# Performance work log

Measured on AMD Instinct MI355X. Metric: run time of the kernel, lower is better.

## Reference

```python
import jax, jax.numpy as jnp
import numpy as np

D_MODEL = 768
EXPAND = 2
D_STATE = 128
HEADDIM = 64
D_CONV = 4
D_INNER = EXPAND * D_MODEL            # 1536
NHEADS = D_INNER // HEADDIM           # 24
CONV_DIM = D_INNER + 2 * D_STATE      # 1792
D_IN_PROJ = 2 * D_INNER + 2 * D_STATE + NHEADS  # 3352
EPS = 1e-5
BATCH, SEQLEN = 2, 2048


def silu(v):
    return v * jax.nn.sigmoid(v)


def mamba2(x, in_w, conv_w, conv_b, dt_bias, A_log, Dp, norm_w, out_w):
    # x: (b, l, d_model)
    b, l, _ = x.shape
    zxbcdt = x @ in_w.T                              # (b, l, d_in_proj)
    z = zxbcdt[..., :D_INNER]
    xBC = zxbcdt[..., D_INNER:D_INNER + CONV_DIM]
    dt = jax.nn.softplus(zxbcdt[..., D_INNER + CONV_DIM:] + dt_bias)  # (b, l, h)
    # causal depthwise conv1d, kernel D_CONV, left padding D_CONV-1
    pad = jnp.pad(xBC, ((0, 0), (D_CONV - 1, 0), (0, 0)))
    conv = conv_b
    for k in range(D_CONV):
        conv = conv + pad[:, k:k + l, :] * conv_w[:, k]
    xBC = silu(conv)
    xh = xBC[..., :D_INNER].reshape(b, l, NHEADS, HEADDIM)   # (b,l,h,p)
    Bm = xBC[..., D_INNER:D_INNER + D_STATE]                 # (b,l,n) ngroups=1
    Cm = xBC[..., D_INNER + D_STATE:]                        # (b,l,n)
    A = -jnp.exp(A_log)                                      # (h,)
    dA = jnp.exp(dt * A)                                     # (b,l,h)

    def step(h, inp):
        dA_t, dt_t, x_t, B_t, C_t = inp
        # h: (b, h, p, n)
        h = h * dA_t[:, :, None, None] + (dt_t[:, :, None] * x_t)[..., None] * B_t[:, None, None, :]
        y = jnp.einsum('bhpn,bn->bhp', h, C_t)
        return h, y

    h0 = jnp.zeros((b, NHEADS, HEADDIM, D_STATE), x.dtype)
    xs = (dA.transpose(1, 0, 2), dt.transpose(1, 0, 2), xh.transpose(1, 0, 2, 3),
          Bm.transpose(1, 0, 2), Cm.transpose(1, 0, 2))
    _, ys = jax.lax.scan(step, h0, xs)                       # (l,b,h,p)
    y = ys.transpose(1, 0, 2, 3) + Dp[None, None, :, None] * xh
    y = y.reshape(b, l, D_INNER)
    # RMSNormGated (norm_before_gate=False): rmsnorm(y * silu(z)) * weight
    y = y * silu(z)
    y = y * jax.lax.rsqrt(jnp.mean(jnp.square(y), axis=-1, keepdims=True) + EPS) * norm_w
    return y @ out_w.T


def setup_inputs() -> dict:
    key = jax.random.key(0)
    ks = jax.random.split(key, 9)
    s = 0.02
    return {
        'x': jax.random.normal(ks[0], (BATCH, SEQLEN, D_MODEL), jnp.float32),
        'in_proj_w': jax.random.normal(ks[1], (2, D_IN_PROJ, D_MODEL), jnp.float32) * s,
        'conv_w': jax.random.normal(ks[2], (2, CONV_DIM, D_CONV), jnp.float32) * 0.2,
        'conv_b': jax.random.normal(ks[3], (2, CONV_DIM), jnp.float32) * s,
        'dt_bias': jax.random.normal(ks[4], (2, NHEADS), jnp.float32) * 0.1,
        'A_log': jnp.log(jax.random.uniform(ks[5], (2, NHEADS), jnp.float32, 1.0, 16.0)),
        'D': jax.random.normal(ks[6], (2, NHEADS), jnp.float32) * 0.5 + 1.0,
        'norm_w': jnp.ones((2, D_INNER), jnp.float32),
        'out_proj_w': jax.random.normal(ks[7], (2, D_MODEL, D_INNER), jnp.float32) * s,
    }


def reference(x, in_proj_w, conv_w, conv_b, dt_bias, A_log, D, norm_w, out_proj_w):
    h_fwd = mamba2(x, in_proj_w[0], conv_w[0], conv_b[0], dt_bias[0], A_log[0], D[0], norm_w[0], out_proj_w[0])
    x_rev = jnp.flip(x, axis=1)
    h_bwd_rev = mamba2(x_rev, in_proj_w[1], conv_w[1], conv_b[1], dt_bias[1], A_log[1], D[1], norm_w[1], out_proj_w[1])
    return h_fwd + jnp.flip(h_bwd_rev, axis=1)
```

## Files before the change

### kernel.cpp

```cpp
#include <hip/hip_runtime.h>
#include <hip/hip_bf16.h>

typedef __attribute__((ext_vector_type(8))) short short8;
typedef __attribute__((ext_vector_type(4))) short bfx4;
typedef __attribute__((ext_vector_type(4))) float floatx4;

#define SEQ     2048
#define DMODEL  768
#define DINNER  1536
#define DSTATE  128
#define NH      24
#define CONVDIM 1792
#define NPROJ   3352
#define QCH     64
#define NCH     (SEQ / QCH)

__device__ inline float bf2f(short s) {
    return __uint_as_float(((unsigned)(unsigned short)s) << 16);
}
__device__ inline short f2bf(float f) {
    __hip_bfloat16 h = __float2bfloat16(f);
    return *reinterpret_cast<short*>(&h);
}
__device__ inline void gl_lds16(const void* g, void* l) {
    __builtin_amdgcn_global_load_lds((const __attribute__((address_space(1))) unsigned int*)g,
                                     (__attribute__((address_space(3))) unsigned int*)l, 16, 0, 0);
}

__global__ __launch_bounds__(256) void cvt_kernel(const float* __restrict__ src,
                                                  __hip_bfloat16* __restrict__ dst, int n4) {
    int i = blockIdx.x * 256 + threadIdx.x;
    if (i >= n4) return;
    float4 v = *(const float4*)(src + (size_t)i * 4);
    bfx4 o = { f2bf(v.x), f2bf(v.y), f2bf(v.z), f2bf(v.w) };
    *(bfx4*)((short*)dst + (size_t)i * 4) = o;
}

__global__ __launch_bounds__(256) void gemm_bt(const __hip_bfloat16* __restrict__ Abase, size_t aStride,
                                               const __hip_bfloat16* __restrict__ Bbase, size_t bStride,
                                               float* __restrict__ C,
                                               __hip_bfloat16* __restrict__ Zb,
                                               __hip_bfloat16* __restrict__ Xb,
                                               float* __restrict__ DT,
                                               float* __restrict__ LA,
                                               const float* __restrict__ dtbias,
                                               const float* __restrict__ Alog,
                                               int M, int N, int K, int zdiv, int mode, int flipA) {
    __shared__ short As[2][64 * 64];
    __shared__ short Bs[2][64 * 64];
    int tid = threadIdx.x;
    int w = tid >> 6, lane = tid & 63;
    int q = lane >> 4, mm = lane & 15;
    int wm = w >> 1, wn = w & 1;
    int m0 = blockIdx.x * 128, n0 = blockIdx.y * 128;
    int z = blockIdx.z;
    int dir = z / zdiv, ks = z - dir * zdiv;
    int kl = K / zdiv;
    int kbeg = ks * kl;
    const short* Ag = (const short*)Abase + (size_t)dir * aStride;
    const short* Bg = (const short*)Bbase + (size_t)dir * bStride;
    int fA = flipA && dir;

    size_t aoff[2], boff[2];
    int ldso[2];
#pragma unroll
    for (int j = 0; j < 2; j++) {
        int widx = w * 2 + j;
        int ln = widx * 8 + (lane >> 3);
        int s  = lane & 7;
        int c  = s ^ (ln & 7);
        int row = (c < 4) ? ln : ln + 64;
        int ch  = (c < 4) ? c : (c ^ 4);
        int ar = m0 + row;
        if (fA) { int bb = ar >> 11, tt = ar & 2047; ar = (bb << 11) + (2047 - tt); }
        aoff[j] = (size_t)ar * K + ch * 8;
        int br = n0 + row; if (br > N - 1) br = N - 1;
        boff[j] = (size_t)br * K + ch * 8;
        ldso[j] = widx * 1024;
    }

    floatx4 acc[16];
#pragma unroll
    for (int i = 0; i < 16; i++) acc[i] = (floatx4){0.f, 0.f, 0.f, 0.f};

    int niter = kl / 32;
    auto stage = [&](int buf, int k0) {
#pragma unroll
        for (int j = 0; j < 2; j++) {
            gl_lds16(Ag + aoff[j] + kbeg + k0, (char*)&As[buf][0] + ldso[j]);
            gl_lds16(Bg + boff[j] + kbeg + k0, (char*)&Bs[buf][0] + ldso[j]);
        }
    };
    stage(0, 0);
    int slotA = (q ^ (mm & 7) ^ (wm << 2)) * 8;
    int slotB = (q ^ (mm & 7) ^ (wn << 2)) * 8;
    for (int it = 0; it < niter; it++) {
        __syncthreads();
        if (it + 1 < niter) stage((it + 1) & 1, (it + 1) * 32);
        const short* Ab = &As[it & 1][0];
        const short* Bb = &Bs[it & 1][0];
        short8 af[4], bfr[4];
#pragma unroll
        for (int mb = 0; mb < 4; mb++)
            af[mb] = *(const short8*)&Ab[(mb * 16 + mm) * 64 + slotA];
#pragma unroll
        for (int nb = 0; nb < 4; nb++)
            bfr[nb] = *(const short8*)&Bb[(nb * 16 + mm) * 64 + slotB];
#pragma unroll
        for (int mb = 0; mb < 4; mb++)
#pragma unroll
            for (int nb = 0; nb < 4; nb++)
                acc[mb * 4 + nb] = __builtin_amdgcn_mfma_f32_16x16x32_bf16(af[mb], bfr[nb], acc[mb * 4 + nb], 0, 0, 0);
    }

    __hip_bfloat16* Zb2 = Zb + (size_t)dir * 4096 * DINNER;
    __hip_bfloat16* Xb2 = Xb + (size_t)dir * 4096 * CONVDIM;
    float* DT2 = DT + (size_t)dir * 4096 * NH;
    float* LA2 = LA + (size_t)dir * 4096 * NH;
    const float* dtb2 = dtbias + dir * NH;
    const float* Al2  = Alog + dir * NH;

#pragma unroll
    for (int mb = 0; mb < 4; mb++) {
#pragma unroll
        for (int nb = 0; nb < 4; nb++) {
            int col = n0 + wn * 64 + nb * 16 + mm;
            if (col >= N) continue;
#pragma unroll
            for (int r = 0; r < 4; r++) {
                int rr = m0 + wm * 64 + mb * 16 + q * 4 + r;
                float v = acc[mb * 4 + nb][r];
                if (mode == 1) {
                    int orow = rr;
                    if (dir) { int b = rr >> 11, t = rr & 2047; orow = (b << 11) + (2047 - t); }
                    atomicAdd(&C[(size_t)orow * N + col], v);
                } else {
                    if (col < DINNER) {
                        Zb2[(size_t)rr * DINNER + col] = __float2bfloat16(v);
                    } else if (col < DINNER + CONVDIM) {
                        Xb2[(size_t)rr * CONVDIM + (col - DINNER)] = __float2bfloat16(v);
                    } else {
                        int hh = col - (DINNER + CONVDIM);
                        float raw = v + dtb2[hh];
                        float dtv = (raw > 20.f) ? raw : log1pf(__expf(raw));
                        float Av  = -__expf(Al2[hh]);
                        DT2[(size_t)rr * NH + hh] = dtv;
                        LA2[(size_t)rr * NH + hh] = dtv * Av;
                    }
                }
            }
        }
    }
}

__global__ __launch_bounds__(256) void conv_kernel(const __hip_bfloat16* __restrict__ Xb,
                                                   const float* __restrict__ conv_w,
                                                   const float* __restrict__ conv_b,
                                                   __hip_bfloat16* __restrict__ xh,
                                                   __hip_bfloat16* __restrict__ Bm,
                                                   __hip_bfloat16* __restrict__ Cm) {
    int db  = blockIdx.x >> 7;
    int dir = db >> 1;
    int t0  = (blockIdx.x & 127) * 16;
    int c8  = threadIdx.x * 8;
    if (c8 >= CONVDIM) return;

    float wk[4][8], bs[8];
#pragma unroll
    for (int j = 0; j < 8; j++) {
        bs[j] = conv_b[dir * CONVDIM + c8 + j];
#pragma unroll
        for (int k = 0; k < 4; k++) wk[k][j] = conv_w[((size_t)dir * CONVDIM + c8 + j) * 4 + k];
    }

    const short* xrow = (const short*)Xb + (size_t)db * SEQ * CONVDIM + c8;
    short8 win[4];
    const short8 zer = {0, 0, 0, 0, 0, 0, 0, 0};
#pragma unroll
    for (int k = 0; k < 3; k++) {
        int ts = t0 - 3 + k;
        win[k] = (ts >= 0) ? *(const short8*)(xrow + (size_t)ts * CONVDIM) : zer;
    }

    for (int tt = 0; tt < 16; tt++) {
        int t = t0 + tt;
        win[3] = *(const short8*)(xrow + (size_t)t * CONVDIM);
        short8 outv;
#pragma unroll
        for (int j = 0; j < 8; j++) {
            float acc = bs[j];
#pragma unroll
            for (int k = 0; k < 4; k++) acc += wk[k][j] * bf2f(win[k][j]);
            float sv = acc / (1.f + __expf(-acc));
            outv[j] = f2bf(sv);
        }
        if (c8 < DINNER)
            *(short8*)((short*)xh + (size_t)(db * SEQ + t) * DINNER + c8) = outv;
        else if (c8 < DINNER + DSTATE)
            *(short8*)((short*)Bm + (size_t)(db * SEQ + t) * DSTATE + (c8 - DINNER)) = outv;
        else
            *(short8*)((short*)Cm + (size_t)(db * SEQ + t) * DSTATE + (c8 - DINNER - DSTATE)) = outv;
        win[0] = win[1]; win[1] = win[2]; win[2] = win[3];
    }
}

__global__ __launch_bounds__(256) void ssd1_kernel(const __hip_bfloat16* __restrict__ XH,
                                                   const __hip_bfloat16* __restrict__ BMh,
                                                   const float* __restrict__ DT,
                                                   const float* __restrict__ LA,
                                                   short* __restrict__ SS,
                                                   float* __restrict__ CUM) {
    int blk = blockIdx.x;
    int ck = blk & 31;
    int dbh = blk >> 5;
    int hh = dbh % NH, db = dbh / NH;
    int base_row = db * SEQ + ck * QCH;

    __shared__ float cum_s[QCH], dt_s[QCH];
    __shared__ short Xt[64][72];
    __shared__ short Bt[128][72];

    int tid = threadIdx.x;
    int lane = tid & 63, w = tid >> 6;
    int q = lane >> 4, mm = lane & 15;

    if (tid < QCH) {
        float la  = LA[(size_t)(base_row + tid) * NH + hh];
        float dtv = DT[(size_t)(base_row + tid) * NH + hh];
        float cs = la;
#pragma unroll
        for (int d = 1; d < 64; d <<= 1) {
            float u = __shfl_up(cs, d);
            if (tid >= d) cs += u;
        }
        cum_s[tid] = cs;
        dt_s[tid] = dtv;
        CUM[(size_t)dbh * SEQ + ck * QCH + tid] = cs;
    }
    __syncthreads();
    float cumL = cum_s[QCH - 1];

    {
        int s2 = (tid & 31) * 2, pb = tid >> 5;
        float f0 = dt_s[s2]     * __expf(cumL - cum_s[s2]);
        float f1 = dt_s[s2 + 1] * __expf(cumL - cum_s[s2 + 1]);
        const short* r0 = (const short*)XH + (size_t)(base_row + s2) * DINNER + hh * 64 + pb * 8;
        const short* r1 = r0 + DINNER;
        short8 x0 = *(const short8*)r0;
        short8 x1 = *(const short8*)r1;
#pragma unroll
        for (int j = 0; j < 8; j++) {
            unsigned lo = (unsigned short)f2bf(f0 * bf2f(x0[j]));
            unsigned hi = (unsigned short)f2bf(f1 * bf2f(x1[j]));
            *(unsigned*)&Xt[pb * 8 + j][s2] = lo | (hi << 16);
        }
    }
    {
        int s2 = (tid & 31) * 2, nb = tid >> 5;
        const short* r0 = (const short*)BMh + (size_t)(base_row + s2) * DSTATE + nb * 16;
        const short* r1 = r0 + DSTATE;
        short8 b0a = *(const short8*)r0,  b0b = *(const short8*)(r0 + 8);
        short8 b1a = *(const short8*)r1,  b1b = *(const short8*)(r1 + 8);
#pragma unroll
        for (int j = 0; j < 8; j++) {
            *(unsigned*)&Bt[nb * 16 + j][s2] =
                (unsigned)(unsigned short)b0a[j] | ((unsigned)(unsigned short)b1a[j] << 16);
            *(unsigned*)&Bt[nb * 16 + 8 + j][s2] =
                (unsigned)(unsigned short)b0b[j] | ((unsigned)(unsigned short)b1b[j] << 16);
        }
    }
    __syncthreads();

    floatx4 acc[8];
#pragma unroll
    for (int i = 0; i < 8; i++) acc[i] = (floatx4){0.f, 0.f, 0.f, 0.f};
#pragma unroll
    for (int kk = 0; kk < 2; kk++) {
        short8 a = *(const short8*)&Xt[w * 16 + mm][kk * 32 + q * 8];
#pragma unroll
        for (int cb = 0; cb < 8; cb++) {
            short8 b = *(const short8*)&Bt[cb * 16 + mm][kk * 32 + q * 8];
            acc[cb] = __builtin_amdgcn_mfma_f32_16x16x32_bf16(a, b, acc[cb], 0, 0, 0);
        }
    }
    short* Sp = SS + (size_t)blk * 8192;
#pragma unroll
    for (int cb = 0; cb < 8; cb++)
#pragma unroll
        for (int r = 0; r < 4; r++)
            Sp[(w * 16 + q * 4 + r) * DSTATE + cb * 16 + mm] = f2bf(acc[cb][r]);
}

__global__ __launch_bounds__(256) void ssd2_kernel(const short* __restrict__ SS,
                                                   const float* __restrict__ CUM,
                                                   short* __restrict__ Hprev) {
    int blk = blockIdx.x;
    int dbh = blk >> 2, part = blk & 3;
    int off = part * 2048 + threadIdx.x * 8;
    size_t base = (size_t)dbh * NCH * 8192 + off;
    float h[8];
#pragma unroll
    for (int j = 0; j < 8; j++) h[j] = 0.f;
    for (int c = 0; c < NCH; c++) {
        float W = __expf(CUM[(size_t)dbh * SEQ + c * QCH + QCH - 1]);
        size_t p = base + (size_t)c * 8192;
        short8 s = *(const short8*)(SS + p);
        short8 o;
#pragma unroll
        for (int j = 0; j < 8; j++) o[j] = f2bf(h[j]);
        *(short8*)(Hprev + p) = o;
#pragma unroll
        for (int j = 0; j < 8; j++) h[j] = fmaf(h[j], W, bf2f(s[j]));
    }
}

__global__ __launch_bounds__(256) void ssd3_kernel(const __hip_bfloat16* __restrict__ XH,
                                                   const __hip_bfloat16* __restrict__ BMh,
                                                   const __hip_bfloat16* __restrict__ CMh,
                                                   const float* __restrict__ DT,
                                                   const float* __restrict__ CUM,
                                                   const short* __restrict__ Hprev,
                                                   __hip_bfloat16* __restrict__ Yb) {
    int blk = blockIdx.x;
    int ck = blk & 31;
    int dbh = blk >> 5;
    int hh = dbh % NH, db = dbh / NH;
    int base_row = db * SEQ + ck * QCH;

    __shared__ float cum_s[QCH], dt_s[QCH];
    __shared__ short Ct[64][136];
    __shared__ short G[64][72];
    __shared__ short Xt[64][72];

    int tid = threadIdx.x;
    int lane = tid & 63, w = tid >> 6;
    int q = lane >> 4, mm = lane & 15;

    if (tid < QCH) {
        cum_s[tid] = CUM[(size_t)dbh * SEQ + ck * QCH + tid];
        dt_s[tid]  = DT[(size_t)(base_row + tid) * NH + hh];
    }

    const short* Cg = (const short*)CMh + (size_t)base_row * DSTATE;
    const short* Bg = (const short*)BMh + (size_t)base_row * DSTATE;
    floatx4 P[4];
#pragma unroll
    for (int i = 0; i < 4; i++) P[i] = (floatx4){0.f, 0.f, 0.f, 0.f};
#pragma unroll
    for (int kk = 0; kk < 4; kk++) {
        short8 a = *(const short8*)(Cg + (size_t)(w * 16 + mm) * DSTATE + kk * 32 + q * 8);
#pragma unroll
        for (int cb = 0; cb < 4; cb++) {
            short8 b = *(const short8*)(Bg + (size_t)(cb * 16 + mm) * DSTATE + kk * 32 + q * 8);
            P[cb] = __builtin_amdgcn_mfma_f32_16x16x32_bf16(a, b, P[cb], 0, 0, 0);
        }
    }
    __syncthreads();

    {
        int t = tid & 63, nb4 = tid >> 6;
        float wt = __expf(cum_s[t]);
        const short* src = Cg + (size_t)t * DSTATE + nb4 * 32;
#pragma unroll
        for (int u = 0; u < 2; u++) {
            short8 v = *(const short8*)(src + u * 16);
            short8 v2 = *(const short8*)(src + u * 16 + 8);
#pragma unroll
            for (int j = 0; j < 4; j++) {
                unsigned lo = (unsigned short)f2bf(wt * bf2f(v[2 * j]));
                unsigned hi = (unsigned short)f2bf(wt * bf2f(v[2 * j + 1]));
                *(unsigned*)&Ct[t][nb4 * 32 + u * 16 + 2 * j] = lo | (hi << 16);
                lo = (unsigned short)f2bf(wt * bf2f(v2[2 * j]));
                hi = (unsigned short)f2bf(wt * bf2f(v2[2 * j + 1]));
                *(unsigned*)&Ct[t][nb4 * 32 + u * 16 + 8 + 2 * j] = lo | (hi << 16);
            }
        }
    }
    {
        int s2 = (tid & 31) * 2, pb = tid >> 5;
        const short* r0 = (const short*)XH + (size_t)(base_row + s2) * DINNER + hh * 64 + pb * 8;
        const short* r1 = r0 + DINNER;
        short8 x0 = *(const short8*)r0;
        short8 x1 = *(const short8*)r1;
#pragma unroll
        for (int j = 0; j < 8; j++) {
            *(unsigned*)&Xt[pb * 8 + j][s2] =
                (unsigned)(unsigned short)x0[j] | ((unsigned)(unsigned short)x1[j] << 16);
        }
    }
#pragma unroll
    for (int cb = 0; cb < 4; cb++) {
#pragma unroll
        for (int r = 0; r < 4; r++) {
            int t = w * 16 + q * 4 + r;
            int s = cb * 16 + mm;
            float g = (s <= t) ? P[cb][r] * __expf(cum_s[t] - cum_s[s]) * dt_s[s] : 0.f;
            G[t][s] = f2bf(g);
        }
    }
    __syncthreads();

    floatx4 Y[4];
#pragma unroll
    for (int i = 0; i < 4; i++) Y[i] = (floatx4){0.f, 0.f, 0.f, 0.f};
#pragma unroll
    for (int kk = 0; kk < 2; kk++) {
        short8 a = *(const short8*)&G[w * 16 + mm][kk * 32 + q * 8];
#pragma unroll
        for (int cb = 0; cb < 4; cb++) {
            short8 b = *(const short8*)&Xt[cb * 16 + mm][kk * 32 + q * 8];
            Y[cb] = __builtin_amdgcn_mfma_f32_16x16x32_bf16(a, b, Y[cb], 0, 0, 0);
        }
    }
    const short* Hc = Hprev + (size_t)blk * 8192;
#pragma unroll
    for (int kk = 0; kk < 4; kk++) {
        short8 a = *(const short8*)&Ct[w * 16 + mm][kk * 32 + q * 8];
#pragma unroll
        for (int cb = 0; cb < 4; cb++) {
            short8 b = *(const short8*)(Hc + (size_t)(cb * 16 + mm) * DSTATE + kk * 32 + q * 8);
            Y[cb] = __builtin_amdgcn_mfma_f32_16x16x32_bf16(a, b, Y[cb], 0, 0, 0);
        }
    }
#pragma unroll
    for (int cb = 0; cb < 4; cb++)
#pragma unroll
        for (int r = 0; r < 4; r++)
            Yb[(size_t)(base_row + w * 16 + q * 4 + r) * DINNER + hh * 64 + cb * 16 + mm] =
                __float2bfloat16(Y[cb][r]);
}

__global__ __launch_bounds__(192) void gate_kernel(const __hip_bfloat16* __restrict__ Yb,
                                                   const __hip_bfloat16* __restrict__ xh,
                                                   const __hip_bfloat16* __restrict__ Zb,
                                                   const float* __restrict__ Dp,
                                                   const float* __restrict__ norm_w,
                                                   __hip_bfloat16* __restrict__ A2) {
    int row = blockIdx.x;
    int dir = row >> 12;
    int c8 = threadIdx.x * 8;
    int hd = c8 >> 6;
    const short* yr = (const short*)Yb + (size_t)row * DINNER + c8;
    const short* xr = (const short*)xh + (size_t)row * DINNER + c8;
    const short* zr = (const short*)Zb + (size_t)row * DINNER + c8;

    short8 y8 = *(const short8*)yr;
    short8 x8 = *(const short8*)xr;
    short8 z8 = *(const short8*)zr;
    float Dv = Dp[dir * NH + hd];

    float vals[8];
    float ss = 0.f;
#pragma unroll
    for (int j = 0; j < 8; j++) {
        float v = bf2f(y8[j]) + Dv * bf2f(x8[j]);
        float z = bf2f(z8[j]);
        v *= z / (1.f + __expf(-z));
        vals[j] = v;
        ss += v * v;
    }
#pragma unroll
    for (int off = 32; off; off >>= 1) ss += __shfl_down(ss, off);
    __shared__ float ls[3];
    if ((threadIdx.x & 63) == 0) ls[threadIdx.x >> 6] = ss;
    __syncthreads();
    float tot = ls[0] + ls[1] + ls[2];
    float scale = rsqrtf(tot / (float)DINNER + 1e-5f);

    const float* nw = norm_w + dir * DINNER + c8;
    short8 o;
#pragma unroll
    for (int j = 0; j < 8; j++) o[j] = f2bf(vals[j] * scale * nw[j]);
    *(short8*)((short*)A2 + (size_t)row * DINNER + c8) = o;
}

extern "C" void kernel_launch(void* const* d_in, const int* in_sizes, int n_in,
                              void* d_out, int out_size, void* d_ws, size_t ws_size,
                              hipStream_t stream) {
    const float* x        = (const float*)d_in[0];
    const float* in_w     = (const float*)d_in[1];
    const float* conv_w   = (const float*)d_in[2];
    const float* conv_b   = (const float*)d_in[3];
    const float* dt_bias  = (const float*)d_in[4];
    const float* A_log    = (const float*)d_in[5];
    const float* Dp       = (const float*)d_in[6];
    const float* norm_w   = (const float*)d_in[7];
    const float* out_w    = (const float*)d_in[8];
    float* out = (float*)d_out;

    const size_t szW2 = (size_t)2 * DMODEL * DINNER * 2;
    const size_t szZ  = (size_t)8192 * DINNER * 2;
    const size_t szXH = (size_t)8192 * DINNER * 2;
    const size_t szBM = (size_t)8192 * DSTATE * 2;
    const size_t szCM = szBM;
    const size_t szDT = (size_t)8192 * NH * 4;
    const size_t szLA = szDT;
    const size_t szA1 = (size_t)4096 * DMODEL * 2;
    const size_t szW1 = (size_t)2 * NPROJ * DMODEL * 2;
    const size_t szXB = (size_t)8192 * CONVDIM * 2;
    const size_t szYb = (size_t)8192 * DINNER * 2;
    const size_t szSS = (size_t)96 * NCH * 8192 * 2;
    const size_t szRa = szA1 + szW1 + szXB;
    size_t szR = szRa;
    if (szR < szYb) szR = szYb;
    if (szR < szSS) szR = szSS;
    const size_t szHp = szSS;
    const size_t szCU = (size_t)96 * SEQ * 4;

    char* ws = (char*)d_ws;
    size_t off = 0;
    auto alloc = [&](size_t bytes) { char* p = ws + off; off += (bytes + 255) & ~(size_t)255; return p; };

    __hip_bfloat16* W2 = (__hip_bfloat16*)alloc(szW2);
    __hip_bfloat16* Z  = (__hip_bfloat16*)alloc(szZ);
    __hip_bfloat16* XH = (__hip_bfloat16*)alloc(szXH);
    __hip_bfloat16* BM = (__hip_bfloat16*)alloc(szBM);
    __hip_bfloat16* CM = (__hip_bfloat16*)alloc(szCM);
    float* DT = (float*)alloc(szDT);
    float* LA = (float*)alloc(szLA);
    char*  R  = (char*)alloc(szR);
    __hip_bfloat16* A1  = (__hip_bfloat16*)R;
    __hip_bfloat16* W1  = (__hip_bfloat16*)(R + szA1);
    __hip_bfloat16* XBC = (__hip_bfloat16*)(R + szA1 + szW1);
    short* SS = (short*)R;
    __hip_bfloat16* Yb = (__hip_bfloat16*)R;

    short* Hp = (short*)alloc(szHp);
    float* CU = (float*)alloc(szCU);
    if (off > ws_size) return;

    int n1 = 2 * NPROJ * DMODEL / 4;
    cvt_kernel<<<(n1 + 255) / 256, 256, 0, stream>>>(in_w, W1, n1);
    int n2 = 2 * DMODEL * DINNER / 4;
    cvt_kernel<<<(n2 + 255) / 256, 256, 0, stream>>>(out_w, W2, n2);
    int n3 = 4096 * DMODEL / 4;
    cvt_kernel<<<(n3 + 255) / 256, 256, 0, stream>>>(x, A1, n3);

    {
        dim3 grid(4096 / 128, (NPROJ + 127) / 128, 2);
        gemm_bt<<<grid, 256, 0, stream>>>(A1, 0,
                                          W1, (size_t)NPROJ * DMODEL,
                                          nullptr, Z, XBC, DT, LA, dt_bias, A_log,
                                          4096, NPROJ, DMODEL, 1, 2, 1);
    }

    conv_kernel<<<4 * 128, 256, 0, stream>>>(XBC, conv_w, conv_b, XH, BM, CM);

    ssd1_kernel<<<4 * NH * NCH, 256, 0, stream>>>(XH, BM, DT, LA, SS, CU);
    ssd2_kernel<<<4 * NH * 4, 256, 0, stream>>>(SS, CU, Hp);
    ssd3_kernel<<<4 * NH * NCH, 256, 0, stream>>>(XH, BM, CM, DT, CU, Hp, Yb);

    gate_kernel<<<2 * 4096, 192, 0, stream>>>(Yb, XH, Z, Dp, norm_w, Z);

    hipMemsetAsync(out, 0, (size_t)4096 * DMODEL * 4, stream);
    {
        dim3 grid(4096 / 128, DMODEL / 128, 4);
        gemm_bt<<<grid, 256, 0, stream>>>(Z, (size_t)4096 * DINNER,
                                          W2, (size_t)DMODEL * DINNER,
                                          out, nullptr, nullptr, nullptr, nullptr, nullptr, nullptr,
                                          4096, DMODEL, DINNER, 2, 1, 0);
    }
}
```

Measured before the change: 386.4 us.

## Replace 128x128 GEMM with 256x256 tile, 512-thread, phased-pipeline kernel

Swaps the 128x128-tile, 256-thread bf16 MFMA GEMM for a 256x256-tile, 512-thread kernel that uses K=64 stages. Each stage is split into four quarter-tile phases, and each phase overlaps its global-to-LDS loads with MFMA work through explicit vmcnt waits, barriers and s_setprio. Both the input and output projections use it. The larger tiles are meant to raise data reuse per LDS load and hide load latency better. In exchange the grids get much smaller (the output projection launches fewer blocks than there are CUs), the kernel needs 128KB of LDS, and more of the padded N range for the input projection is wasted work.

New measurement: 437.1 us. 13.1% more time.

```diff
diff --git a/kernel.cpp b/kernel.cpp
--- a/kernel.cpp
+++ b/kernel.cpp
@@ -36,116 +36,162 @@
     *(bfx4*)((short*)dst + (size_t)i * 4) = o;
 }
 
-__global__ __launch_bounds__(256) void gemm_bt(const __hip_bfloat16* __restrict__ Abase, size_t aStride,
-                                               const __hip_bfloat16* __restrict__ Bbase, size_t bStride,
-                                               float* __restrict__ C,
-                                               __hip_bfloat16* __restrict__ Zb,
-                                               __hip_bfloat16* __restrict__ Xb,
-                                               float* __restrict__ DT,
-                                               float* __restrict__ LA,
-                                               const float* __restrict__ dtbias,
-                                               const float* __restrict__ Alog,
-                                               int M, int N, int K, int zdiv, int mode, int flipA) {
-    __shared__ short As[2][64 * 64];
-    __shared__ short Bs[2][64 * 64];
+#define GPHASE(AH, BH, WAITC, STAGEC) do {                                      \
+    WAITC;                                                                       \
+    __builtin_amdgcn_s_barrier();                                                \
+    __builtin_amdgcn_sched_barrier(0);                                           \
+    STAGEC;                                                                      \
+    const short* Au0 = &As[dbuf][AH][0][0];                                      \
+    const short* Au1 = &As[dbuf][AH][1][0];                                      \
+    const short* Bu0 = &Bs[dbuf][BH][0][0];                                      \
+    const short* Bu1 = &Bs[dbuf][BH][1][0];                                      \
+    short8 af0[4], af1[4], bq0[2], bq1[2];                                       \
+    _Pragma("unroll")                                                            \
+    for (int mi = 0; mi < 4; mi++) {                                             \
+        af0[mi] = *(const short8*)&Au0[aRd[mi]];                                 \
+        af1[mi] = *(const short8*)&Au1[aRd[mi]];                                 \
+    }                                                                            \
+    _Pragma("unroll")                                                            \
+    for (int ni = 0; ni < 2; ni++) {                                             \
+        bq0[ni] = *(const short8*)&Bu0[bRd[ni]];                                 \
+        bq1[ni] = *(const short8*)&Bu1[bRd[ni]];                                 \
+    }                                                                            \
+    __builtin_amdgcn_s_setprio(1);                                               \
+    _Pragma("unroll")                                                            \
+    for (int mi = 0; mi < 4; mi++)                                               \
+    _Pragma("unroll")                                                            \
+    for (int ni = 0; ni < 2; ni++) {                                             \
+        acc[(((AH)*2+(BH))*4+mi)*2+ni] = __builtin_amdgcn_mfma_f32_16x16x32_bf16(\
+            af0[mi], bq0[ni], acc[(((AH)*2+(BH))*4+mi)*2+ni], 0, 0, 0);          \
+        acc[(((AH)*2+(BH))*4+mi)*2+ni] = __builtin_amdgcn_mfma_f32_16x16x32_bf16(\
+            af1[mi], bq1[ni], acc[(((AH)*2+(BH))*4+mi)*2+ni], 0, 0, 0);          \
+    }                                                                            \
+    __builtin_amdgcn_s_setprio(0);                                               \
+} while (0)
+
+__global__ __launch_bounds__(512, 2) void gemm256(const __hip_bfloat16* __restrict__ Abase, size_t aStride,
+                                                  const __hip_bfloat16* __restrict__ Bbase, size_t bStride,
+                                                  float* __restrict__ C,
+                                                  __hip_bfloat16* __restrict__ Zb,
+                                                  __hip_bfloat16* __restrict__ Xb,
+                                                  float* __restrict__ DT,
+                                                  float* __restrict__ LA,
+                                                  const float* __restrict__ dtbias,
+                                                  const float* __restrict__ Alog,
+                                                  int M, int N, int K, int zdiv, int mode, int flipA) {
+    __shared__ short As[2][2][2][4096];
+    __shared__ short Bs[2][2][2][4096];
     int tid = threadIdx.x;
     int w = tid >> 6, lane = tid & 63;
     int q = lane >> 4, mm = lane & 15;
-    int wm = w >> 1, wn = w & 1;
-    int m0 = blockIdx.x * 128, n0 = blockIdx.y * 128;
+    int wm = w >> 2, wn = w & 3;
+    int m0 = blockIdx.x * 256, n0 = blockIdx.y * 256;
     int z = blockIdx.z;
     int dir = z / zdiv, ks = z - dir * zdiv;
-    int kl = K / zdiv;
-    int kbeg = ks * kl;
+    int kl = K / zdiv, kbeg = ks * kl;
+    int nkt = kl / 64;
     const short* Ag = (const short*)Abase + (size_t)dir * aStride;
     const short* Bg = (const short*)Bbase + (size_t)dir * bStride;
     int fA = flipA && dir;
 
+    int ln   = w * 8 + (lane >> 3);
+    int sl   = lane & 7;
+    int cc   = sl ^ (ln & 7);
+    int lrow = (cc < 4) ? ln : ln + 64;
+    int chk  = (cc < 4) ? cc : (cc ^ 4);
+    int wbase = w * 512;
     size_t aoff[2], boff[2];
-    int ldso[2];
-#pragma unroll
-    for (int j = 0; j < 2; j++) {
-        int widx = w * 2 + j;
-        int ln = widx * 8 + (lane >> 3);
-        int s  = lane & 7;
-        int c  = s ^ (ln & 7);
-        int row = (c < 4) ? ln : ln + 64;
-        int ch  = (c < 4) ? c : (c ^ 4);
-        int ar = m0 + row;
+#pragma unroll
+    for (int h = 0; h < 2; h++) {
+        int ar = m0 + h * 128 + lrow;
         if (fA) { int bb = ar >> 11, tt = ar & 2047; ar = (bb << 11) + (2047 - tt); }
-        aoff[j] = (size_t)ar * K + ch * 8;
-        int br = n0 + row; if (br > N - 1) br = N - 1;
-        boff[j] = (size_t)br * K + ch * 8;
-        ldso[j] = widx * 1024;
-    }
-
-    floatx4 acc[16];
-#pragma unroll
-    for (int i = 0; i < 16; i++) acc[i] = (floatx4){0.f, 0.f, 0.f, 0.f};
-
-    int niter = kl / 32;
-    auto stage = [&](int buf, int k0) {
-#pragma unroll
-        for (int j = 0; j < 2; j++) {
-            gl_lds16(Ag + aoff[j] + kbeg + k0, (char*)&As[buf][0] + ldso[j]);
-            gl_lds16(Bg + boff[j] + kbeg + k0, (char*)&Bs[buf][0] + ldso[j]);
-        }
+        aoff[h] = (size_t)ar * K + chk * 8;
+        int br = n0 + h * 128 + lrow; if (br > N - 1) br = N - 1;
+        boff[h] = (size_t)br * K + chk * 8;
+    }
+
+    int slotA = (q ^ (mm & 7) ^ (wm << 2)) * 8;
+    int slotB = (q ^ (mm & 7) ^ ((wn >> 1) << 2)) * 8;
+    int aRd[4], bRd[2];
+#pragma unroll
+    for (int mi = 0; mi < 4; mi++) aRd[mi] = (mi * 16 + mm) * 64 + slotA;
+#pragma unroll
+    for (int ni = 0; ni < 2; ni++) bRd[ni] = ((wn & 1) * 32 + ni * 16 + mm) * 64 + slotB;
+
+    floatx4 acc[32];
+#pragma unroll
+    for (int i = 0; i < 32; i++) acc[i] = (floatx4){0.f, 0.f, 0.f, 0.f};
+
+    auto stageA = [&](int kt2, int h) {
+        int d = kt2 & 1;
+        const short* s0 = Ag + aoff[h] + kbeg + kt2 * 64;
+        gl_lds16(s0,      &As[d][h][0][wbase]);
+        gl_lds16(s0 + 32, &As[d][h][1][wbase]);
     };
-    stage(0, 0);
-    int slotA = (q ^ (mm & 7) ^ (wm << 2)) * 8;
-    int slotB = (q ^ (mm & 7) ^ (wn << 2)) * 8;
-    for (int it = 0; it < niter; it++) {
-        __syncthreads();
-        if (it + 1 < niter) stage((it + 1) & 1, (it + 1) * 32);
-        const short* Ab = &As[it & 1][0];
-        const short* Bb = &Bs[it & 1][0];
-        short8 af[4], bfr[4];
-#pragma unroll
-        for (int mb = 0; mb < 4; mb++)
-            af[mb] = *(const short8*)&Ab[(mb * 16 + mm) * 64 + slotA];
-#pragma unroll
-        for (int nb = 0; nb < 4; nb++)
-            bfr[nb] = *(const short8*)&Bb[(nb * 16 + mm) * 64 + slotB];
-#pragma unroll
-        for (int mb = 0; mb < 4; mb++)
-#pragma unroll
-            for (int nb = 0; nb < 4; nb++)
-                acc[mb * 4 + nb] = __builtin_amdgcn_mfma_f32_16x16x32_bf16(af[mb], bfr[nb], acc[mb * 4 + nb], 0, 0, 0);
+    auto stageB = [&](int kt2, int h) {
+        int d = kt2 & 1;
+        const short* s0 = Bg + boff[h] + kbeg + kt2 * 64;
+        gl_lds16(s0,      &Bs[d][h][0][wbase]);
+        gl_lds16(s0 + 32, &Bs[d][h][1][wbase]);
+    };
+
+    stageA(0, 0); stageB(0, 0);
+    stageA(0, 1); stageB(0, 1);
+    if (nkt > 1) { stageA(1, 0); stageB(1, 0); }
+
+    for (int kt = 0; kt < nkt; kt++) {
+        int dbuf = kt & 1;
+        GPHASE(0, 0,
+            { if (kt + 1 < nkt) asm volatile("s_waitcnt vmcnt(8)" ::: "memory");
+              else              asm volatile("s_waitcnt vmcnt(4)" ::: "memory"); },
+            { if (kt + 1 < nkt) stageA(kt + 1, 1); });
+        GPHASE(0, 1,
+            { if (kt + 1 < nkt) asm volatile("s_waitcnt vmcnt(6)" ::: "memory");
+              else              asm volatile("s_waitcnt vmcnt(0)" ::: "memory"); },
+            { if (kt + 1 < nkt) stageB(kt + 1, 1); });
+        GPHASE(1, 0, { }, { if (kt + 2 < nkt) stageA(kt + 2, 0); });
+        GPHASE(1, 1, { }, { if (kt + 2 < nkt) stageB(kt + 2, 0); });
     }
 
     __hip_bfloat16* Zb2 = Zb + (size_t)dir * 4096 * DINNER;
     __hip_bfloat16* Xb2 = Xb + (size_t)dir * 4096 * CONVDIM;
     float* DT2 = DT + (size_t)dir * 4096 * NH;
     float* LA2 = LA + (size_t)dir * 4096 * NH;
-    const float* dtb2 = dtbias + dir * NH;
-    const float* Al2  = Alog + dir * NH;
-
-#pragma unroll
-    for (int mb = 0; mb < 4; mb++) {
-#pragma unroll
-        for (int nb = 0; nb < 4; nb++) {
-            int col = n0 + wn * 64 + nb * 16 + mm;
-            if (col >= N) continue;
-#pragma unroll
-            for (int r = 0; r < 4; r++) {
-                int rr = m0 + wm * 64 + mb * 16 + q * 4 + r;
-                float v = acc[mb * 4 + nb][r];
-                if (mode == 1) {
-                    int orow = rr;
-                    if (dir) { int b = rr >> 11, t = rr & 2047; orow = (b << 11) + (2047 - t); }
-                    atomicAdd(&C[(size_t)orow * N + col], v);
-                } else {
-                    if (col < DINNER) {
-                        Zb2[(size_t)rr * DINNER + col] = __float2bfloat16(v);
-                    } else if (col < DINNER + CONVDIM) {
-                        Xb2[(size_t)rr * CONVDIM + (col - DINNER)] = __float2bfloat16(v);
-                    } else {
-                        int hh = col - (DINNER + CONVDIM);
-                        float raw = v + dtb2[hh];
-                        float dtv = (raw > 20.f) ? raw : log1pf(__expf(raw));
-                        float Av  = -__expf(Al2[hh]);
-                        DT2[(size_t)rr * NH + hh] = dtv;
-                        LA2[(size_t)rr * NH + hh] = dtv * Av;
+    const float* dtb2 = dtbias ? dtbias + dir * NH : nullptr;
+    const float* Al2  = Alog ? Alog + dir * NH : nullptr;
+
+#pragma unroll
+    for (int Ah = 0; Ah < 2; Ah++) {
+#pragma unroll
+        for (int Bh = 0; Bh < 2; Bh++) {
+#pragma unroll
+            for (int mi = 0; mi < 4; mi++) {
+#pragma unroll
+                for (int ni = 0; ni < 2; ni++) {
+                    int col = n0 + Bh * 128 + wn * 32 + ni * 16 + mm;
+                    if (col >= N) continue;
+#pragma unroll
+                    for (int r = 0; r < 4; r++) {
+                        int rr = m0 + Ah * 128 + wm * 64 + mi * 16 + q * 4 + r;
+                        float v = acc[((Ah * 2 + Bh) * 4 + mi) * 2 + ni][r];
+                        if (mode == 1) {
+                            int orow = rr;
+                            if (dir) { int b = rr >> 11, t = rr & 2047; orow = (b << 11) + (2047 - t); }
+                            atomicAdd(&C[(size_t)orow * N + col], v);
+                        } else {
+                            if (col < DINNER) {
+                                Zb2[(size_t)rr * DINNER + col] = __float2bfloat16(v);
+                            } else if (col < DINNER + CONVDIM) {
+                                Xb2[(size_t)rr * CONVDIM + (col - DINNER)] = __float2bfloat16(v);
+                            } else {
+                                int hh = col - (DINNER + CONVDIM);
+                                float raw = v + dtb2[hh];
+                                float dtv = (raw > 20.f) ? raw : log1pf(__expf(raw));
+                                float Av  = -__expf(Al2[hh]);
+                                DT2[(size_t)rr * NH + hh] = dtv;
+                                LA2[(size_t)rr * NH + hh] = dtv * Av;
+                            }
+                        }
                     }
                 }
             }
@@ -537,8 +583,8 @@
     cvt_kernel<<<(n3 + 255) / 256, 256, 0, stream>>>(x, A1, n3);
 
     {
-        dim3 grid(4096 / 128, (NPROJ + 127) / 128, 2);
-        gemm_bt<<<grid, 256, 0, stream>>>(A1, 0,
+        dim3 grid(4096 / 256, (NPROJ + 255) / 256, 2);
+        gemm256<<<grid, 512, 0, stream>>>(A1, 0,
                                           W1, (size_t)NPROJ * DMODEL,
                                           nullptr, Z, XBC, DT, LA, dt_bias, A_log,
                                           4096, NPROJ, DMODEL, 1, 2, 1);
@@ -554,8 +600,8 @@
 
     hipMemsetAsync(out, 0, (size_t)4096 * DMODEL * 4, stream);
     {
-        dim3 grid(4096 / 128, DMODEL / 128, 4);
-        gemm_bt<<<grid, 256, 0, stream>>>(Z, (size_t)4096 * DINNER,
+        dim3 grid(4096 / 256, DMODEL / 256, 4);
+        gemm256<<<grid, 512, 0, stream>>>(Z, (size_t)4096 * DINNER,
                                           W2, (size_t)DMODEL * DINNER,
                                           out, nullptr, nullptr, nullptr, nullptr, nullptr, nullptr,
                                           4096, DMODEL, DINNER, 2, 1, 0);
```
